# Optimization experiments

Measured on AMD Instinct MI355X. Metric: run time of the kernel, lower is better.

Reference implementation:

```python
import jax, jax.numpy as jnp
import numpy as np

# DeformConv (RegSeg): offset conv + mask conv (sigmoid) + modulated deformable conv v2
STRIDE = 1
PAD = 1
DIL = 1
G = 1          # deformable_groups
KH, KW = 3, 3


def _conv(x, w, b):
    # standard NCHW conv, stride/pad/dilation of the module
    y = jax.lax.conv_general_dilated(
        x, w, window_strides=(STRIDE, STRIDE),
        padding=((PAD, PAD), (PAD, PAD)), rhs_dilation=(DIL, DIL),
        dimension_numbers=("NCHW", "OIHW", "NCHW"))
    return y + b[None, :, None, None]


def _deform_conv2d(x, offset, mask, w, b):
    # torchvision DeformConv2d (modulated, v2) semantics
    B, C, H, W = x.shape
    O = w.shape[0]
    K = KH * KW
    Ho = (H + 2 * PAD - DIL * (KH - 1) - 1) // STRIDE + 1
    Wo = (W + 2 * PAD - DIL * (KW - 1) - 1) // STRIDE + 1
    Cg = C // G

    # base sampling grid: p0 + p_k
    ky = jnp.repeat(jnp.arange(KH), KW) * DIL            # [K]
    kx = jnp.tile(jnp.arange(KW), KH) * DIL              # [K]
    oy = jnp.arange(Ho) * STRIDE - PAD                   # [Ho]
    ox = jnp.arange(Wo) * STRIDE - PAD                   # [Wo]
    base_y = (ky[:, None, None] + oy[None, :, None]).astype(x.dtype)  # [K,Ho,1]
    base_x = (kx[:, None, None] + ox[None, None, :]).astype(x.dtype)  # [K,1,Wo]

    off = offset.reshape(B, G, K, 2, Ho, Wo)             # channel layout: g, k, (dy,dx)
    py = base_y[None, None] + off[:, :, :, 0]            # [B,G,K,Ho,Wo]
    px = base_x[None, None] + off[:, :, :, 1]
    m = mask.reshape(B, G, K, Ho, Wo)

    imgf = x.reshape(B * G, Cg, H * W)
    y0 = jnp.floor(py).astype(jnp.int32)
    x0 = jnp.floor(px).astype(jnp.int32)
    ly = py - y0.astype(x.dtype)
    lx = px - x0.astype(x.dtype)

    def corner(iy, ix, wgt):
        # zero-padded bilinear corner: out-of-bounds corners contribute 0
        valid = (iy >= 0) & (iy < H) & (ix >= 0) & (ix < W)
        idx = (jnp.clip(iy, 0, H - 1) * W + jnp.clip(ix, 0, W - 1)).reshape(B * G, -1)
        g = jax.vmap(lambda im, ii: im[:, ii])(imgf, idx)            # [B*G,Cg,K*Ho*Wo]
        g = g.reshape(B, G, Cg, K, Ho, Wo)
        return g * (wgt * valid.astype(x.dtype))[:, :, None]          # [B,G,Cg,K,Ho,Wo]

    val = (corner(y0,     x0,     (1 - ly) * (1 - lx))
         + corner(y0,     x0 + 1, (1 - ly) * lx)
         + corner(y0 + 1, x0,     ly * (1 - lx))
         + corner(y0 + 1, x0 + 1, ly * lx))
    val = val * m[:, :, None]                                         # modulation

    wr = w.reshape(O, G, Cg, K)
    out = jnp.einsum("bgckpq,ogck->bopq", val, wr) + b[None, :, None, None]
    return out


def setup_inputs() -> dict:
    key = jax.random.key(0)
    ks = jax.random.split(key, 8)
    B, C, H, W, O = 4, 128, 96, 96, 128
    K = KH * KW
    fan = 1.0 / np.sqrt(C * K)
    return {
        "x":        jax.random.normal(ks[0], (B, C, H, W), jnp.float32),
        "x2":       jax.random.normal(ks[1], (B, C, H, W), jnp.float32),
        "offset_w": jax.random.normal(ks[2], (2 * G * K, C, KH, KW), jnp.float32) * 0.01,
        "offset_b": jax.random.normal(ks[3], (2 * G * K,), jnp.float32) * 0.01,
        "mask_w":   jax.random.normal(ks[4], (G * K, C, KH, KW), jnp.float32) * 0.05,
        "mask_b":   jnp.zeros((G * K,), jnp.float32),
        "deform_w": jax.random.normal(ks[5], (O, C, KH, KW), jnp.float32) * fan,
        "deform_b": jax.random.normal(ks[6], (O,), jnp.float32) * fan,
    }


def reference(x, x2, offset_w, offset_b, mask_w, mask_b, deform_w, deform_b):
    offset = _conv(x2, offset_w, offset_b)
    mask = jax.nn.sigmoid(_conv(x2, mask_w, mask_b))
    return _deform_conv2d(x, offset, mask, deform_w, deform_b)
```

## Files before the change

kernel.cpp:

```cpp
#include <hip/hip_runtime.h>

#define CIN   128
#define HH    96
#define WW    96
#define OUTC  128
#define HWSZ  9216
#define KK    9
#define KTOT  1152

typedef __bf16 bf16x8 __attribute__((ext_vector_type(8)));
typedef float  f32x4  __attribute__((ext_vector_type(4)));

__device__ __forceinline__ unsigned short f2bf(float f) {
  unsigned u = __builtin_bit_cast(unsigned, f);
  u += 0x7fffu + ((u >> 16) & 1u);
  return (unsigned short)(u >> 16);
}
__device__ __forceinline__ float bf2f_lo(unsigned w) {
  unsigned u = w << 16;
  return __builtin_bit_cast(float, u);
}
__device__ __forceinline__ float bf2f_hi(unsigned w) {
  unsigned u = w & 0xffff0000u;
  return __builtin_bit_cast(float, u);
}
__device__ __forceinline__ unsigned pack_bf(float v0, float v1) {
  unsigned u0 = __builtin_bit_cast(unsigned, v0) + 0x8000u;
  unsigned u1 = __builtin_bit_cast(unsigned, v1) + 0x8000u;
  return __builtin_amdgcn_perm(u1, u0, 0x07060302u);
}

#define WT2T_O 147456
#define BIAS_O 184320
#define XN_O   184384
#define X2N_O  (184384 + 4718592)

__global__ __launch_bounds__(256) void prep_all(
    const float* __restrict__ x, const float* __restrict__ x2,
    const float* __restrict__ offw, const float* __restrict__ maskw,
    const float* __restrict__ defw, const float* __restrict__ offb,
    const float* __restrict__ maskb, void* __restrict__ wsv) {
  int bid = blockIdx.x;
  int t = threadIdx.x;
  if (bid < 1152) {
    __shared__ unsigned short tile[64][138];
    int tsel = bid / 576;
    int rem = bid - tsel * 576;
    int b = rem / 144;
    int hw0 = (rem % 144) * 64;
    const float* src = tsel ? x2 : x;
    unsigned short* dst = (unsigned short*)wsv + (tsel ? X2N_O : XN_O);
    int px = t & 63, cg = t >> 6;
#pragma unroll
    for (int q = 0; q < 16; ++q) {
      int c = cg * 32 + 2 * q;
      float f0 = src[((size_t)(b * CIN + c))     * HWSZ + hw0 + px];
      float f1 = src[((size_t)(b * CIN + c + 1)) * HWSZ + hw0 + px];
      *(unsigned*)&tile[px][c] = pack_bf(f0, f1);
    }
    __syncthreads();
    unsigned* drow = (unsigned*)(dst + ((size_t)(b * HWSZ + hw0)) * 128);
#pragma unroll
    for (int k = 0; k < 16; ++k) {
      int e = t + 256 * k;
      int pxx = e >> 6, j = e & 63;
      unsigned v = *(const unsigned*)&tile[pxx][2 * j];
      drow[(size_t)pxx * 64 + j] = v;
    }
    return;
  }
  unsigned short* wtt  = (unsigned short*)wsv;
  unsigned short* wt2t = wtt + WT2T_O;
  float* bias32 = (float*)(wtt + BIAS_O);
  int idx = (bid - 1152) * 256 + t;
  if (idx < OUTC * KTOT) {
    int o = idx / KTOT, r = idx - o * KTOT;
    int c = r / KK, tap = r - c * KK;
    int nt = o >> 4, l15o = o & 15;
    int ks = c >> 5, quad = (c >> 3) & 3, j = c & 7;
    wtt[(size_t)(((tap * 4 + ks) * 8 + nt) * 64 + quad * 16 + l15o) * 8 + j] =
        f2bf(defw[idx]);
  } else if (idx < OUTC * KTOT + 32 * KTOT) {
    int jj = idx - OUTC * KTOT;
    int oc = jj / KTOT, r = jj - oc * KTOT;
    int c = r / KK, tap = r - c * KK;
    float v = 0.f;
    if (oc < 18)      v = offw[jj];
    else if (oc < 27) v = maskw[jj - 18 * KTOT];
    int nt2 = oc >> 4, l15o = oc & 15;
    int ks = c >> 5, quad = (c >> 3) & 3, j = c & 7;
    wt2t[(size_t)(((tap * 4 + ks) * 2 + nt2) * 64 + quad * 16 + l15o) * 8 + j] =
        f2bf(v);
  } else if (idx < OUTC * KTOT + 32 * KTOT + 32) {
    int j = idx - OUTC * KTOT - 32 * KTOT;
    float v = 0.f;
    if (j < 18) v = offb[j]; else if (j < 27) v = maskb[j - 18];
    bias32[j] = v;
  }
}

__global__ __launch_bounds__(256, 3) void fused(
    const float* __restrict__ defb, const void* __restrict__ wsv,
    float* __restrict__ out) {
  const unsigned short* wtt  = (const unsigned short*)wsv;
  const unsigned short* wt2t = wtt + WT2T_O;
  const float* bias32 = (const float*)(wtt + BIAS_O);
  const unsigned short* xn  = wtt + XN_O;
  const unsigned short* x2n = wtt + X2N_O;

  __shared__ unsigned short val[64][144];
  __shared__ float om[32][68];
  __shared__ unsigned sidxw[KK * 4 * 64];

  int t = threadIdx.x;
  int w = t >> 6;
  int l = t & 63;
  int l15 = l & 15, quad = l >> 4;
  int rb = blockIdx.x;
  int bid = (rb & 7) * 72 + (rb >> 3);
  int b = bid / 144;
  int pblk = (bid % 144) * 64;

  int phg[4], pwg[4];
#pragma unroll
  for (int G = 0; G < 4; ++G) {
    int p = pblk + w * 16 + G * 4 + quad;
    phg[G] = p / WW;
    pwg[G] = p - phg[G] * WW;
  }

  f32x4 oa0 = {0.f, 0.f, 0.f, 0.f};
  f32x4 oa1 = {0.f, 0.f, 0.f, 0.f};
  const unsigned short* x2nb = x2n + ((size_t)b * HWSZ) * 128;
  for (int tap = 0; tap < KK; ++tap) {
    int ky = tap / 3 - 1, kx = tap % 3 - 1;
#pragma unroll
    for (int G = 0; G < 4; ++G) {
      int y = phg[G] + ky, xx = pwg[G] + kx;
      bool ok = ((unsigned)y < HH) && ((unsigned)xx < WW);
      int pos = ok ? (y * WW + xx) : 0;
      uint4 v = *(const uint4*)(x2nb + ((size_t)pos << 7) + l15 * 8);
      if (!ok) v = make_uint4(0u, 0u, 0u, 0u);
      *(uint4*)&val[w * 16 + G * 4 + quad][l15 * 8] = v;
    }
#pragma unroll
    for (int ks = 0; ks < 4; ++ks) {
      bf16x8 af = *(const bf16x8*)&val[w * 16 + l15][ks * 32 + quad * 8];
      const unsigned short* bp = wt2t + (size_t)(((tap * 4 + ks) * 2) * 64 + l) * 8;
      bf16x8 b0 = *(const bf16x8*)bp;
      bf16x8 b1 = *(const bf16x8*)(bp + 64 * 8);
      oa0 = __builtin_amdgcn_mfma_f32_16x16x32_bf16(af, b0, oa0, 0, 0, 0);
      oa1 = __builtin_amdgcn_mfma_f32_16x16x32_bf16(af, b1, oa1, 0, 0, 0);
    }
  }
#pragma unroll
  for (int nt = 0; nt < 2; ++nt) {
    f32x4 a = nt ? oa1 : oa0;
    int oc = nt * 16 + l15;
    float bia = bias32[oc];
#pragma unroll
    for (int r = 0; r < 4; ++r)
      om[oc][w * 16 + quad * 4 + r] = a[r] + bia;
  }
  __syncthreads();

  for (int e = t; e < KK * 64; e += 256) {
    int tap = e >> 6, pp = e & 63;
    int gp2 = pblk + pp;
    int h = gp2 / WW, ww_ = gp2 % WW;
    float dy = om[2 * tap][pp], dx = om[2 * tap + 1][pp];
    float mr = om[18 + tap][pp];
    float m = 1.f / (1.f + __expf(-mr));
    float py  = (float)(h + tap / 3 - 1) + dy;
    float pxx = (float)(ww_ + tap % 3 - 1) + dx;
    float y0f = floorf(py), x0f = floorf(pxx);
    int y0 = (int)y0f, x0 = (int)x0f;
    float ly = py - y0f, lx = pxx - x0f;
    int y1 = y0 + 1, x1 = x0 + 1;
    bool vy0 = (unsigned)y0 < HH, vy1 = (unsigned)y1 < HH;
    bool vx0 = (unsigned)x0 < WW, vx1 = (unsigned)x1 < WW;
    int cy0 = min(max(y0, 0), HH - 1), cy1 = min(max(y1, 0), HH - 1);
    int cx0 = min(max(x0, 0), WW - 1), cx1 = min(max(x1, 0), WW - 1);
    unsigned i00 = cy0 * WW + cx0, i01 = cy0 * WW + cx1;
    unsigned i10 = cy1 * WW + cx0, i11 = cy1 * WW + cx1;
    float w00 = (vy0 && vx0) ? m * (1.f - ly) * (1.f - lx) : 0.f;
    float w01 = (vy0 && vx1) ? m * (1.f - ly) * lx         : 0.f;
    float w10 = (vy1 && vx0) ? m * ly * (1.f - lx)         : 0.f;
    float w11 = (vy1 && vx1) ? m * ly * lx                 : 0.f;
    sidxw[(tap * 4 + 0) * 64 + pp] = i00 | ((unsigned)f2bf(w00) << 16);
    sidxw[(tap * 4 + 1) * 64 + pp] = i01 | ((unsigned)f2bf(w01) << 16);
    sidxw[(tap * 4 + 2) * 64 + pp] = i10 | ((unsigned)f2bf(w10) << 16);
    sidxw[(tap * 4 + 3) * 64 + pp] = i11 | ((unsigned)f2bf(w11) << 16);
  }
  __syncthreads();

  f32x4 acc[8];
#pragma unroll
  for (int nt = 0; nt < 8; ++nt) acc[nt] = (f32x4){0.f, 0.f, 0.f, 0.f};
  const unsigned short* xnb = xn + ((size_t)b * HWSZ) * 128;

  for (int tap = 0; tap < KK; ++tap) {
    unsigned sw[4][4];
#pragma unroll
    for (int cr = 0; cr < 4; ++cr)
#pragma unroll
      for (int G = 0; G < 4; ++G)
        sw[cr][G] = sidxw[(tap * 4 + cr) * 64 + w * 16 + G * 4 + quad];
    uint4 v[4][4];
#pragma unroll
    for (int G = 0; G < 4; ++G)
#pragma unroll
      for (int cr = 0; cr < 4; ++cr)
        v[cr][G] = *(const uint4*)(xnb + ((size_t)(sw[cr][G] & 0xffffu) << 7) + l15 * 8);
#pragma unroll
    for (int G = 0; G < 4; ++G) {
      float f[8];
#pragma unroll
      for (int j = 0; j < 8; ++j) f[j] = 0.f;
#pragma unroll
      for (int cr = 0; cr < 4; ++cr) {
        float wc = bf2f_hi(sw[cr][G]);
        const unsigned* a = (const unsigned*)&v[cr][G];
#pragma unroll
        for (int j = 0; j < 4; ++j) {
          f[2 * j]     += wc * bf2f_lo(a[j]);
          f[2 * j + 1] += wc * bf2f_hi(a[j]);
        }
      }
      unsigned od[4];
#pragma unroll
      for (int j = 0; j < 4; ++j) od[j] = pack_bf(f[2 * j], f[2 * j + 1]);
      *(uint4*)&val[w * 16 + G * 4 + quad][l15 * 8] =
          make_uint4(od[0], od[1], od[2], od[3]);
    }
    bf16x8 af[4];
#pragma unroll
    for (int ks = 0; ks < 4; ++ks)
      af[ks] = *(const bf16x8*)&val[w * 16 + l15][ks * 32 + quad * 8];
#pragma unroll
    for (int ks = 0; ks < 4; ++ks) {
      const unsigned short* bp = wtt + (size_t)(((tap * 4 + ks) * 8) * 64 + l) * 8;
#pragma unroll
      for (int nt = 0; nt < 8; ++nt) {
        bf16x8 bb = *(const bf16x8*)(bp + (size_t)nt * 64 * 8);
        acc[nt] = __builtin_amdgcn_mfma_f32_16x16x32_bf16(af[ks], bb, acc[nt], 0, 0, 0);
      }
    }
  }

  for (int r = 0; r < 4; ++r) {
    f32x4 a0 = acc[2 * r], a1 = acc[2 * r + 1];
    float db0 = defb[r * 32 + l15];
    float db1 = defb[r * 32 + 16 + l15];
    if (r) __syncthreads();
#pragma unroll
    for (int reg = 0; reg < 4; ++reg) {
      om[l15]     [w * 16 + quad * 4 + reg] = a0[reg] + db0;
      om[16 + l15][w * 16 + quad * 4 + reg] = a1[reg] + db1;
    }
    __syncthreads();
    int row = t >> 4;
    int col4 = (t & 15) * 4;
#pragma unroll
    for (int hrow = 0; hrow < 2; ++hrow) {
      int rr = row + hrow * 16;
      float4 vv = *(float4*)&om[rr][col4];
      *(float4*)&out[((size_t)b * OUTC + r * 32 + rr) * HWSZ + pblk + col4] = vv;
    }
  }
}

extern "C" void kernel_launch(void* const* d_in, const int* in_sizes, int n_in,
                              void* d_out, int out_size, void* d_ws, size_t ws_size,
                              hipStream_t stream) {
  const float* x     = (const float*)d_in[0];
  const float* x2    = (const float*)d_in[1];
  const float* offw  = (const float*)d_in[2];
  const float* offb  = (const float*)d_in[3];
  const float* maskw = (const float*)d_in[4];
  const float* maskb = (const float*)d_in[5];
  const float* defw  = (const float*)d_in[6];
  const float* defb  = (const float*)d_in[7];
  float* out = (float*)d_out;

  hipLaunchKernelGGL(prep_all, dim3(1873), dim3(256), 0, stream,
                     x, x2, offw, maskw, defw, offb, maskb, d_ws);
  hipLaunchKernelGGL(fused, dim3(576), dim3(256), 0, stream, defb, d_ws, out);
}
```

Before: 165.2 us.

## Stage offset-conv input bands in LDS and prefetch gather/weights per tap

The offset/mask conv now loads a contiguous band of 66 pixel rows of x2 per kernel row into swizzled shared memory. Each band is reused across the three horizontal taps and the next band is prefetched in registers. The deformable stage software-pipelines the next tap's bilinear gathers and its 128x128 weight slice, and stages the weights in LDS so they are not re-read from global memory per wave. This is meant to cut redundant global loads and hide gather latency, but it raises LDS use (about 32KB for weights) and register pressure, so launch bounds drop from 3 to 2 blocks per SM.

```diff
diff --git a/kernel.cpp b/kernel.cpp
--- a/kernel.cpp
+++ b/kernel.cpp
@@ -99,7 +99,10 @@
   }
 }
 
-__global__ __launch_bounds__(256, 3) void fused(
+#define BAND_ROWS 66
+#define BAND_SLOTS (BAND_ROWS * 16)
+
+__global__ __launch_bounds__(256, 2) void fused(
     const float* __restrict__ defb, const void* __restrict__ wsv,
     float* __restrict__ out) {
   const unsigned short* wtt  = (const unsigned short*)wsv;
@@ -108,9 +111,9 @@
   const unsigned short* xn  = wtt + XN_O;
   const unsigned short* x2n = wtt + X2N_O;
 
-  __shared__ unsigned short val[64][144];
-  __shared__ float om[32][68];
-  __shared__ unsigned sidxw[KK * 4 * 64];
+  __shared__ __align__(16) unsigned short sB[16384];
+  __shared__ __align__(16) unsigned valw[BAND_ROWS * 64];
+  __shared__ __align__(16) unsigned omsx[2304];
 
   int t = threadIdx.x;
   int w = t >> 6;
@@ -121,36 +124,69 @@
   int b = bid / 144;
   int pblk = (bid % 144) * 64;
 
-  int phg[4], pwg[4];
-#pragma unroll
-  for (int G = 0; G < 4; ++G) {
-    int p = pblk + w * 16 + G * 4 + quad;
-    phg[G] = p / WW;
-    pwg[G] = p - phg[G] * WW;
-  }
+  int px_m = w * 16 + l15;
+  int gp = pblk + px_m;
+  int pw_m = gp % WW;
+
+  const unsigned short* x2nb = x2n + ((size_t)b * HWSZ) * 128;
+  float* omv = (float*)omsx;
+
+  uint4 brg[5];
+  auto band_load = [&](int ky, uint4* r) {
+#pragma unroll
+    for (int i = 0; i < 5; ++i) {
+      int cc = t + 256 * i;
+      if (cc < BAND_SLOTS) {
+        int row = cc >> 4, c16 = cc & 15;
+        int rr = pblk + (ky - 1) * WW - 1 + row;
+        bool ok = ((unsigned)rr < HWSZ);
+        uint4 v = make_uint4(0u, 0u, 0u, 0u);
+        if (ok) v = *(const uint4*)(x2nb + ((size_t)rr << 7) + c16 * 8);
+        r[i] = v;
+      }
+    }
+  };
+  auto band_store = [&](uint4* r) {
+#pragma unroll
+    for (int i = 0; i < 5; ++i) {
+      int cc = t + 256 * i;
+      if (cc < BAND_SLOTS) {
+        int row = cc >> 4, c16 = cc & 15;
+        *(uint4*)&valw[row * 64 + ((c16 * 4) ^ ((row & 7) << 2))] = r[i];
+      }
+    }
+  };
+
+  band_load(0, brg);
+  band_store(brg);
+  __syncthreads();
 
   f32x4 oa0 = {0.f, 0.f, 0.f, 0.f};
   f32x4 oa1 = {0.f, 0.f, 0.f, 0.f};
-  const unsigned short* x2nb = x2n + ((size_t)b * HWSZ) * 128;
-  for (int tap = 0; tap < KK; ++tap) {
-    int ky = tap / 3 - 1, kx = tap % 3 - 1;
-#pragma unroll
-    for (int G = 0; G < 4; ++G) {
-      int y = phg[G] + ky, xx = pwg[G] + kx;
-      bool ok = ((unsigned)y < HH) && ((unsigned)xx < WW);
-      int pos = ok ? (y * WW + xx) : 0;
-      uint4 v = *(const uint4*)(x2nb + ((size_t)pos << 7) + l15 * 8);
-      if (!ok) v = make_uint4(0u, 0u, 0u, 0u);
-      *(uint4*)&val[w * 16 + G * 4 + quad][l15 * 8] = v;
-    }
-#pragma unroll
-    for (int ks = 0; ks < 4; ++ks) {
-      bf16x8 af = *(const bf16x8*)&val[w * 16 + l15][ks * 32 + quad * 8];
-      const unsigned short* bp = wt2t + (size_t)(((tap * 4 + ks) * 2) * 64 + l) * 8;
-      bf16x8 b0 = *(const bf16x8*)bp;
-      bf16x8 b1 = *(const bf16x8*)(bp + 64 * 8);
-      oa0 = __builtin_amdgcn_mfma_f32_16x16x32_bf16(af, b0, oa0, 0, 0, 0);
-      oa1 = __builtin_amdgcn_mfma_f32_16x16x32_bf16(af, b1, oa1, 0, 0, 0);
+  for (int ky = 0; ky < 3; ++ky) {
+    uint4 nrg[5];
+    if (ky < 2) band_load(ky + 1, nrg);
+#pragma unroll
+    for (int kx = 0; kx < 3; ++kx) {
+      int tap = ky * 3 + kx;
+      bool okx = ((unsigned)(pw_m + kx - 1) < WW);
+      int bi = px_m + kx;
+#pragma unroll
+      for (int ks = 0; ks < 4; ++ks) {
+        int col4 = ks * 16 + quad * 4;
+        bf16x8 af = *(const bf16x8*)&valw[bi * 64 + (col4 ^ ((bi & 7) << 2))];
+        if (!okx) af = (bf16x8){};
+        const unsigned short* bp = wt2t + (size_t)(((tap * 4 + ks) * 2) * 64 + l) * 8;
+        bf16x8 b0 = *(const bf16x8*)bp;
+        bf16x8 b1 = *(const bf16x8*)(bp + 512);
+        oa0 = __builtin_amdgcn_mfma_f32_16x16x32_bf16(af, b0, oa0, 0, 0, 0);
+        oa1 = __builtin_amdgcn_mfma_f32_16x16x32_bf16(af, b1, oa1, 0, 0, 0);
+      }
+    }
+    __syncthreads();
+    if (ky < 2) {
+      band_store(nrg);
+      __syncthreads();
     }
   }
 #pragma unroll
@@ -160,37 +196,49 @@
     float bia = bias32[oc];
 #pragma unroll
     for (int r = 0; r < 4; ++r)
-      om[oc][w * 16 + quad * 4 + r] = a[r] + bia;
+      omv[oc * 64 + w * 16 + quad * 4 + r] = a[r] + bia;
   }
   __syncthreads();
 
-  for (int e = t; e < KK * 64; e += 256) {
-    int tap = e >> 6, pp = e & 63;
-    int gp2 = pblk + pp;
-    int h = gp2 / WW, ww_ = gp2 % WW;
-    float dy = om[2 * tap][pp], dx = om[2 * tap + 1][pp];
-    float mr = om[18 + tap][pp];
-    float m = 1.f / (1.f + __expf(-mr));
-    float py  = (float)(h + tap / 3 - 1) + dy;
-    float pxx = (float)(ww_ + tap % 3 - 1) + dx;
-    float y0f = floorf(py), x0f = floorf(pxx);
-    int y0 = (int)y0f, x0 = (int)x0f;
-    float ly = py - y0f, lx = pxx - x0f;
-    int y1 = y0 + 1, x1 = x0 + 1;
-    bool vy0 = (unsigned)y0 < HH, vy1 = (unsigned)y1 < HH;
-    bool vx0 = (unsigned)x0 < WW, vx1 = (unsigned)x1 < WW;
-    int cy0 = min(max(y0, 0), HH - 1), cy1 = min(max(y1, 0), HH - 1);
-    int cx0 = min(max(x0, 0), WW - 1), cx1 = min(max(x1, 0), WW - 1);
-    unsigned i00 = cy0 * WW + cx0, i01 = cy0 * WW + cx1;
-    unsigned i10 = cy1 * WW + cx0, i11 = cy1 * WW + cx1;
-    float w00 = (vy0 && vx0) ? m * (1.f - ly) * (1.f - lx) : 0.f;
-    float w01 = (vy0 && vx1) ? m * (1.f - ly) * lx         : 0.f;
-    float w10 = (vy1 && vx0) ? m * ly * (1.f - lx)         : 0.f;
-    float w11 = (vy1 && vx1) ? m * ly * lx                 : 0.f;
-    sidxw[(tap * 4 + 0) * 64 + pp] = i00 | ((unsigned)f2bf(w00) << 16);
-    sidxw[(tap * 4 + 1) * 64 + pp] = i01 | ((unsigned)f2bf(w01) << 16);
-    sidxw[(tap * 4 + 2) * 64 + pp] = i10 | ((unsigned)f2bf(w10) << 16);
-    sidxw[(tap * 4 + 3) * 64 + pp] = i11 | ((unsigned)f2bf(w11) << 16);
+  uint4 pkreg[3];
+#pragma unroll
+  for (int i = 0; i < 3; ++i) {
+    int e = t + 256 * i;
+    if (e < KK * 64) {
+      int tap = e >> 6, pp = e & 63;
+      int gp2 = pblk + pp;
+      int h = gp2 / WW, ww_ = gp2 % WW;
+      float dy = omv[(2 * tap) * 64 + pp], dx = omv[(2 * tap + 1) * 64 + pp];
+      float mr = omv[(18 + tap) * 64 + pp];
+      float m = 1.f / (1.f + __expf(-mr));
+      float py  = (float)(h + tap / 3 - 1) + dy;
+      float pxx = (float)(ww_ + tap % 3 - 1) + dx;
+      float y0f = floorf(py), x0f = floorf(pxx);
+      int y0 = (int)y0f, x0 = (int)x0f;
+      float ly = py - y0f, lx = pxx - x0f;
+      int y1 = y0 + 1, x1 = x0 + 1;
+      bool vy0 = (unsigned)y0 < HH, vy1 = (unsigned)y1 < HH;
+      bool vx0 = (unsigned)x0 < WW, vx1 = (unsigned)x1 < WW;
+      int cy0 = min(max(y0, 0), HH - 1), cy1 = min(max(y1, 0), HH - 1);
+      int cx0 = min(max(x0, 0), WW - 1), cx1 = min(max(x1, 0), WW - 1);
+      unsigned i00 = cy0 * WW + cx0, i01 = cy0 * WW + cx1;
+      unsigned i10 = cy1 * WW + cx0, i11 = cy1 * WW + cx1;
+      float w00 = (vy0 && vx0) ? m * (1.f - ly) * (1.f - lx) : 0.f;
+      float w01 = (vy0 && vx1) ? m * (1.f - ly) * lx         : 0.f;
+      float w10 = (vy1 && vx0) ? m * ly * (1.f - lx)         : 0.f;
+      float w11 = (vy1 && vx1) ? m * ly * lx                 : 0.f;
+      pkreg[i].x = i00 | ((unsigned)f2bf(w00) << 16);
+      pkreg[i].y = i01 | ((unsigned)f2bf(w01) << 16);
+      pkreg[i].z = i10 | ((unsigned)f2bf(w10) << 16);
+      pkreg[i].w = i11 | ((unsigned)f2bf(w11) << 16);
+    }
+  }
+  __syncthreads();
+  uint4* prm = (uint4*)omsx;
+#pragma unroll
+  for (int i = 0; i < 3; ++i) {
+    int e = t + 256 * i;
+    if (e < KK * 64) prm[e] = pkreg[i];
   }
   __syncthreads();
 
@@ -199,28 +247,36 @@
   for (int nt = 0; nt < 8; ++nt) acc[nt] = (f32x4){0.f, 0.f, 0.f, 0.f};
   const unsigned short* xnb = xn + ((size_t)b * HWSZ) * 128;
 
+  uint4 pk[4], v[4][4], bB[8];
+  auto issue_tap = [&](int tap) {
+#pragma unroll
+    for (int G = 0; G < 4; ++G)
+      pk[G] = prm[tap * 64 + w * 16 + G * 4 + quad];
+#pragma unroll
+    for (int G = 0; G < 4; ++G) {
+      const unsigned* pc = (const unsigned*)&pk[G];
+#pragma unroll
+      for (int cr = 0; cr < 4; ++cr)
+        v[G][cr] = *(const uint4*)(xnb + ((size_t)(pc[cr] & 0xffffu) << 7) + l15 * 8);
+    }
+    const unsigned short* wsrc = wtt + (size_t)tap * 16384;
+#pragma unroll
+    for (int j = 0; j < 8; ++j)
+      bB[j] = *(const uint4*)(wsrc + (size_t)(j * 256 + t) * 8);
+  };
+
+  issue_tap(0);
   for (int tap = 0; tap < KK; ++tap) {
-    unsigned sw[4][4];
-#pragma unroll
-    for (int cr = 0; cr < 4; ++cr)
-#pragma unroll
-      for (int G = 0; G < 4; ++G)
-        sw[cr][G] = sidxw[(tap * 4 + cr) * 64 + w * 16 + G * 4 + quad];
-    uint4 v[4][4];
-#pragma unroll
-    for (int G = 0; G < 4; ++G)
-#pragma unroll
-      for (int cr = 0; cr < 4; ++cr)
-        v[cr][G] = *(const uint4*)(xnb + ((size_t)(sw[cr][G] & 0xffffu) << 7) + l15 * 8);
 #pragma unroll
     for (int G = 0; G < 4; ++G) {
+      const unsigned* pc = (const unsigned*)&pk[G];
       float f[8];
 #pragma unroll
       for (int j = 0; j < 8; ++j) f[j] = 0.f;
 #pragma unroll
       for (int cr = 0; cr < 4; ++cr) {
-        float wc = bf2f_hi(sw[cr][G]);
-        const unsigned* a = (const unsigned*)&v[cr][G];
+        float wc = bf2f_hi(pc[cr]);
+        const unsigned* a = (const unsigned*)&v[G][cr];
 #pragma unroll
         for (int j = 0; j < 4; ++j) {
           f[2 * j]     += wc * bf2f_lo(a[j]);
@@ -230,24 +286,33 @@
       unsigned od[4];
 #pragma unroll
       for (int j = 0; j < 4; ++j) od[j] = pack_bf(f[2 * j], f[2 * j + 1]);
-      *(uint4*)&val[w * 16 + G * 4 + quad][l15 * 8] =
+      int row = w * 16 + G * 4 + quad;
+      *(uint4*)&valw[row * 64 + ((l15 * 4) ^ ((row & 7) << 2))] =
           make_uint4(od[0], od[1], od[2], od[3]);
     }
+#pragma unroll
+    for (int j = 0; j < 8; ++j)
+      ((uint4*)sB)[j * 256 + t] = bB[j];
+    __syncthreads();
+    if (tap < 8) issue_tap(tap + 1);
     bf16x8 af[4];
 #pragma unroll
+    for (int ks = 0; ks < 4; ++ks) {
+      int row = w * 16 + l15;
+      af[ks] = *(const bf16x8*)&valw[row * 64 +
+                 ((ks * 16 + quad * 4) ^ ((l15 & 7) << 2))];
+    }
+#pragma unroll
     for (int ks = 0; ks < 4; ++ks)
-      af[ks] = *(const bf16x8*)&val[w * 16 + l15][ks * 32 + quad * 8];
-#pragma unroll
-    for (int ks = 0; ks < 4; ++ks) {
-      const unsigned short* bp = wtt + (size_t)(((tap * 4 + ks) * 8) * 64 + l) * 8;
 #pragma unroll
       for (int nt = 0; nt < 8; ++nt) {
-        bf16x8 bb = *(const bf16x8*)(bp + (size_t)nt * 64 * 8);
+        bf16x8 bb = *(const bf16x8*)&sB[(size_t)(((ks * 8 + nt) * 64) + l) * 8];
         acc[nt] = __builtin_amdgcn_mfma_f32_16x16x32_bf16(af[ks], bb, acc[nt], 0, 0, 0);
       }
-    }
-  }
-
+    __syncthreads();
+  }
+
+  float* fb = (float*)omsx;
   for (int r = 0; r < 4; ++r) {
     f32x4 a0 = acc[2 * r], a1 = acc[2 * r + 1];
     float db0 = defb[r * 32 + l15];
@@ -255,8 +320,8 @@
     if (r) __syncthreads();
 #pragma unroll
     for (int reg = 0; reg < 4; ++reg) {
-      om[l15]     [w * 16 + quad * 4 + reg] = a0[reg] + db0;
-      om[16 + l15][w * 16 + quad * 4 + reg] = a1[reg] + db1;
+      fb[l15 * 72        + w * 16 + quad * 4 + reg] = a0[reg] + db0;
+      fb[(16 + l15) * 72 + w * 16 + quad * 4 + reg] = a1[reg] + db1;
     }
     __syncthreads();
     int row = t >> 4;
@@ -264,7 +329,7 @@
 #pragma unroll
     for (int hrow = 0; hrow < 2; ++hrow) {
       int rr = row + hrow * 16;
-      float4 vv = *(float4*)&om[rr][col4];
+      float4 vv = *(float4*)&fb[rr * 72 + col4];
       *(float4*)&out[((size_t)b * OUTC + r * 32 + rr) * HWSZ + pblk + col4] = vv;
     }
   }
```

New measurement: 188.8 us. +14.3%, slower.
